# Optimization experiments

Hardware: AMD Instinct MI355X
Metric: run time of the kernel (lower is better)

The kernel has to match this reference:

```python
import jax, jax.numpy as jnp
import numpy as np

B = 2048; IN_DIM = 60; TTL = 30; H = 512; L = 5; OUT = 23
T_PTS = 90; SUB = 10  # fixed-step RK4 substeps per day (stands in for per-sample dopri5)
P_D = 0.2; P_H = 0.15; P_V = 0.25  # DELPHI fixed detection/hospitalization/ventilation fractions
LN2 = float(np.log(2.0))
R_I = LN2/5.0; R_D = LN2/2.0; R_RI = LN2/10.0; R_RH = LN2/15.0; R_RV = LN2/10.0


def setup_inputs():
    ks = jax.random.split(jax.random.key(0), 24)
    w = lambda k, s: (jax.random.normal(k, s) * 0.05).astype(jnp.float32)
    rng = jnp.array([1.0]*11 + [1.0, 60.0, 4.0, 0.5, 0.3, 0.5, 5.0, 5.0, 2.0, 60.0, 30.0, 1.0], dtype=jnp.float32)
    return {
        'model_input': jax.random.normal(ks[0], (B, IN_DIM), dtype=jnp.float32),
        'population': jax.random.uniform(ks[1], (B,), minval=1e5, maxval=1e7, dtype=jnp.float32),
        'cumulative_case_number': jax.random.uniform(ks[2], (B, 1), minval=1e3, maxval=1e5, dtype=jnp.float32),
        'mortality_rate': jax.random.uniform(ks[3], (B,), minval=0.01, maxval=0.05, dtype=jnp.float32),
        'h0': jax.random.normal(ks[4], (L, B, H), dtype=jnp.float32),
        'c0': jax.random.normal(ks[5], (L, B, H), dtype=jnp.float32),
        'W_ih0': w(ks[6], (4*H, TTL)),
        'W_ihR': w(ks[7], (L-1, 4*H, H)),
        'W_hh': w(ks[8], (L, 4*H, H)),
        'b_ih': w(ks[9], (L, 4*H)),
        'b_hh': w(ks[10], (L, 4*H)),
        'meta_W1': w(ks[11], (H, IN_DIM - TTL)), 'meta_b1': w(ks[12], (H,)),
        'meta_W2': w(ks[13], (H, H)), 'meta_b2': w(ks[14], (H,)),
        'ro_W1': w(ks[15], (2*H, 2*H)), 'ro_b1': w(ks[16], (2*H,)),
        'ro_W2': w(ks[17], (OUT, 2*H)), 'ro_b2': w(ks[18], (OUT,)),
        'dnn_output_range': rng,
        'sigmoid_scale': 1,
    }


def _backbone(model_input, population, h0, c0, W_ih0, W_ihR, W_hh, b_ih, b_hh,
              meta_W1, meta_b1, meta_W2, meta_b2, ro_W1, ro_b1, ro_W2, ro_b2,
              dnn_output_range, sigmoid_scale):
    x = model_input[:, :TTL] / population[:, None]
    for l in range(L):  # single-timestep, 5-layer LSTM; torch gate order i,f,g,o
        Wi = W_ih0 if l == 0 else W_ihR[l-1]
        g = x @ Wi.T + b_ih[l] + h0[l] @ W_hh[l].T + b_hh[l]
        gi, gf, gg, go = jnp.split(g, 4, axis=1)
        c = jax.nn.sigmoid(gf) * c0[l] + jax.nn.sigmoid(gi) * jnp.tanh(gg)
        x = jax.nn.sigmoid(go) * jnp.tanh(c)
    ts_out = x  # [B, H]
    m = jax.nn.relu(model_input[:, TTL:] @ meta_W1.T + meta_b1)
    m = jax.nn.relu(m @ meta_W2.T + meta_b2)
    z = jnp.concatenate([ts_out, m], axis=1)  # [B, 2H]
    z = jnp.tanh(z @ ro_W1.T + ro_b1)
    raw = z @ ro_W2.T + ro_b2  # [B, OUT]
    dnn = jax.nn.sigmoid(raw * sigmoid_scale) * dnn_output_range
    return dnn, ts_out, raw


def _ode(dnn, population, cumulative_case_number, mortality_rate):
    p = dnn[:, 11:]  # 12 fitted DELPHI params per sample
    alpha, days, r_s, r_dth, p_dth, r_dthdecay, k1, k2, jump, t_jump, std_normal, k3 = [p[:, j] for j in range(12)]
    N = population
    PopI = cumulative_case_number[:, 0]
    PopD = jnp.floor(mortality_rate * PopI)
    R_0 = jnp.where(PopI - PopD > 5.0 * PopD, 5.0 * PopD, 0.0)
    PopCI = PopI - PopD - R_0
    # DELPHI initial conditions
    S0 = N - (PopCI/P_D)*(k1 + k2) - R_0/P_D - PopD/P_D
    y0 = jnp.stack([
        S0,
        PopCI/P_D*k1,                      # E
        PopCI/P_D*k2,                      # I
        (PopCI/P_D - PopCI)*(1.0 - p_dth), # AR
        PopCI*P_H*(1.0 - p_dth),           # DHR
        PopCI*(1.0 - P_H)*(1.0 - p_dth),   # DQR
        (PopCI/P_D - PopCI)*p_dth,         # AD
        PopCI*P_H*p_dth,                   # DHD
        PopCI*(1.0 - P_H)*p_dth,           # DQD
        R_0/P_D,                           # R
        PopD/P_D,                          # D
        PopCI*P_H,                         # TH
        PopCI*P_H*P_V*(1.0 - p_dth),       # DVR
        PopCI*P_H*P_V*p_dth,               # DVD
        PopD,                              # DD
        PopI,                              # DT
    ], axis=1)  # [B, 16]

    def deriv(t, y):
        S, E, I = y[:, 0], y[:, 1], y[:, 2]
        AR, DHR, DQR, AD, DHD, DQD = y[:, 3], y[:, 4], y[:, 5], y[:, 6], y[:, 7], y[:, 8]
        DVR, DVD = y[:, 12], y[:, 13]
        gam = (2.0/jnp.pi)*jnp.arctan(-(t - days)/20.0*r_s) + 1.0 \
              + jump*jnp.exp(-(t - t_jump)**2/(2.0*std_normal**2))
        pdt = (2.0/jnp.pi)*(p_dth - 0.001)*(jnp.arctan(-t*r_dthdecay/20.0) + jnp.pi/2.0) + 0.001
        inf = alpha*gam*S*I/N
        det = R_D*I
        return jnp.stack([
            -inf,
            inf - R_I*E,
            R_I*E - det,
            det*(1.0-pdt)*(1.0-P_D) - R_RI*AR,
            det*(1.0-pdt)*P_D*P_H - R_RH*DHR,
            det*(1.0-pdt)*P_D*(1.0-P_H) - R_RI*DQR,
            det*pdt*(1.0-P_D) - r_dth*AD,
            det*pdt*P_D*P_H - r_dth*DHD,
            det*pdt*P_D*(1.0-P_H) - r_dth*DQD,
            R_RI*(AR + DQR) + R_RH*DHR,
            r_dth*(AD + DQD + DHD),
            det*P_D*P_H,
            det*(1.0-pdt)*P_D*P_H*P_V - R_RV*DVR,
            det*pdt*P_D*P_H*P_V - r_dth*DVD,
            r_dth*(DHD + DQD),
            det*P_D,
        ], axis=1)

    dt = 1.0 / SUB

    def segment(y, t0):
        def sub(yy, j):
            t = t0 + j*dt
            k1_ = deriv(t, yy)
            k2_ = deriv(t + 0.5*dt, yy + 0.5*dt*k1_)
            k3_ = deriv(t + 0.5*dt, yy + 0.5*dt*k2_)
            k4_ = deriv(t + dt, yy + dt*k3_)
            return yy + (dt/6.0)*(k1_ + 2.0*k2_ + 2.0*k3_ + k4_), None
        y2, _ = jax.lax.scan(sub, y, jnp.arange(SUB, dtype=jnp.float32))
        return y2, y2

    _, ys = jax.lax.scan(segment, y0, jnp.arange(T_PTS - 1, dtype=jnp.float32))
    sol = jnp.concatenate([y0[None], ys], axis=0)  # [T_PTS, B, 16]
    return jnp.transpose(sol, (1, 0, 2))  # [B, T_PTS, 16]


def reference(model_input, population, cumulative_case_number, mortality_rate, h0, c0,
              W_ih0, W_ihR, W_hh, b_ih, b_hh, meta_W1, meta_b1, meta_W2, meta_b2,
              ro_W1, ro_b1, ro_W2, ro_b2, dnn_output_range, sigmoid_scale):
    dnn, ts_out, raw = _backbone(model_input, population, h0, c0, W_ih0, W_ihR, W_hh,
                                 b_ih, b_hh, meta_W1, meta_b1, meta_W2, meta_b2,
                                 ro_W1, ro_b1, ro_W2, ro_b2, dnn_output_range, sigmoid_scale)
    sol = _ode(dnn, population, cumulative_case_number, mortality_rate)
    return sol, dnn, ts_out[:, None, :], raw
```

## Files before the change

### kernel.cpp

```cpp
#include <hip/hip_runtime.h>
#include <hip/hip_bf16.h>
#include <math.h>

#define BATCH 2048
#define HID 512
#define TPTS 90
#define NSEG 89
#define NSUB 10
#define NSTEPS 890

__device__ __constant__ const float kR_I  = 0.6931471805599453f / 5.0f;
__device__ __constant__ const float kR_D  = 0.6931471805599453f / 2.0f;
__device__ __constant__ const float kR_RI = 0.6931471805599453f / 10.0f;
__device__ __constant__ const float kR_RH = 0.6931471805599453f / 15.0f;
__device__ __constant__ const float kR_RV = 0.6931471805599453f / 10.0f;

typedef __attribute__((ext_vector_type(8))) short short8;
typedef __attribute__((ext_vector_type(4))) short short4v;
typedef __attribute__((ext_vector_type(4))) float float4v;

__device__ __forceinline__ float sigmoidf_(float x) { return 1.0f / (1.0f + expf(-x)); }

__global__ void prep_pad(const float* __restrict__ mi, const float* __restrict__ pop,
                         const float* __restrict__ Wih0, const float* __restrict__ mW1,
                         float* __restrict__ x0p, float* __restrict__ xmp,
                         float* __restrict__ Wp0, float* __restrict__ Wpm)
{
    int i = blockIdx.x * 256 + threadIdx.x;
    int r = i >> 5, c = i & 31;
    bool v = (c < 30);
    x0p[i] = v ? mi[r * 60 + c] / pop[r] : 0.0f;
    xmp[i] = v ? mi[r * 60 + 30 + c] : 0.0f;
    Wp0[i] = v ? Wih0[r * 30 + c] : 0.0f;
    if (r < 512) Wpm[i] = v ? mW1[r * 30 + c] : 0.0f;
}

template<bool WMODE>
__global__ void pack_split4(const float* __restrict__ s1, int ld1, int K1,
                            const float* __restrict__ s2, int ld2, int K2,
                            __hip_bfloat16* __restrict__ dst, int rows)
{
    int idx = blockIdx.x * 256 + threadIdx.x;
    int Ks = K1 + K2, Kq = Ks >> 2;
    if (idx >= rows * Kq) return;
    int r = idx / Kq, k4 = (idx - r * Kq) << 2;
    const float* srcp; int base, seg, kk;
    if (k4 < K1) { srcp = s1 + (size_t)r * ld1 + k4; base = 0; seg = K1; kk = k4; }
    else { kk = k4 - K1; srcp = s2 + (size_t)r * ld2 + kk; base = 3 * K1; seg = K2; }
    float4 x = *(const float4*)srcp;
    union { __hip_bfloat16 b[4]; short4v v; } H, L;
    H.b[0] = __float2bfloat16(x.x); H.b[1] = __float2bfloat16(x.y);
    H.b[2] = __float2bfloat16(x.z); H.b[3] = __float2bfloat16(x.w);
    L.b[0] = __float2bfloat16(x.x - __bfloat162float(H.b[0]));
    L.b[1] = __float2bfloat16(x.y - __bfloat162float(H.b[1]));
    L.b[2] = __float2bfloat16(x.z - __bfloat162float(H.b[2]));
    L.b[3] = __float2bfloat16(x.w - __bfloat162float(H.b[3]));
    __hip_bfloat16* d = dst + (size_t)r * (3 * Ks) + base;
    *(short4v*)(d + kk)           = H.v;
    *(short4v*)(d + seg + kk)     = WMODE ? L.v : H.v;
    *(short4v*)(d + 2 * seg + kk) = WMODE ? H.v : L.v;
}

template<int ACT>
__global__ __launch_bounds__(256)
void gemm_mfma(const __hip_bfloat16* __restrict__ Ah,
               const __hip_bfloat16* __restrict__ Wh, int K3,
               const float* __restrict__ b1, const float* __restrict__ b2,
               float* __restrict__ Cp, int ldc, int N)
{
    __shared__ __hip_bfloat16 As[128 * 32];
    __shared__ __hip_bfloat16 Ws[128 * 32];
    const int tid  = threadIdx.x;
    const int m0   = blockIdx.y * 128;
    const int n0   = blockIdx.x * 128;
    const int lane = tid & 63, wv = tid >> 6;
    const int mw   = (wv >> 1) * 64, nw = (wv & 1) * 64;
    const int l15  = lane & 15, quad = lane >> 4;
    const int sr   = tid >> 2;
    const int sc   = (tid & 3) * 8;

    float4v acc[4][4];
    #pragma unroll
    for (int i = 0; i < 4; ++i)
        #pragma unroll
        for (int j = 0; j < 4; ++j)
            acc[i][j] = (float4v){0.0f, 0.0f, 0.0f, 0.0f};

    const __hip_bfloat16* pa0 = Ah + (size_t)(m0 + sr)      * K3 + sc;
    const __hip_bfloat16* pa1 = Ah + (size_t)(m0 + sr + 64) * K3 + sc;
    const __hip_bfloat16* pw0 = Wh + (size_t)(n0 + sr)      * K3 + sc;
    const __hip_bfloat16* pw1 = Wh + (size_t)(n0 + sr + 64) * K3 + sc;

    short8 a0 = *(const short8*)(pa0);
    short8 a1 = *(const short8*)(pa1);
    short8 w0 = *(const short8*)(pw0);
    short8 w1 = *(const short8*)(pw1);

    for (int kt = 0; kt < K3; kt += 32) {
        __syncthreads();
        *(short8*)(As + sr * 32 + sc)        = a0;
        *(short8*)(As + (sr + 64) * 32 + sc) = a1;
        *(short8*)(Ws + sr * 32 + sc)        = w0;
        *(short8*)(Ws + (sr + 64) * 32 + sc) = w1;
        __syncthreads();

        int kn = kt + 32;
        if (kn < K3) {
            a0 = *(const short8*)(pa0 + kn);
            a1 = *(const short8*)(pa1 + kn);
            w0 = *(const short8*)(pw0 + kn);
            w1 = *(const short8*)(pw1 + kn);
        }

        short8 af[4], bf[4];
        #pragma unroll
        for (int t = 0; t < 4; ++t) {
            af[t] = *(const short8*)(As + (mw + t * 16 + l15) * 32 + quad * 8);
            bf[t] = *(const short8*)(Ws + (nw + t * 16 + l15) * 32 + quad * 8);
        }
        #pragma unroll
        for (int i = 0; i < 4; ++i)
            #pragma unroll
            for (int j = 0; j < 4; ++j)
                acc[i][j] = __builtin_amdgcn_mfma_f32_16x16x32_bf16(af[i], bf[j], acc[i][j], 0, 0, 0);
    }

    #pragma unroll
    for (int j = 0; j < 4; ++j) {
        int col = n0 + nw + j * 16 + l15;
        float bias = b1[col] + (b2 ? b2[col] : 0.0f);
        #pragma unroll
        for (int i = 0; i < 4; ++i) {
            #pragma unroll
            for (int r = 0; r < 4; ++r) {
                int row = m0 + mw + i * 16 + quad * 4 + r;
                float v = acc[i][j][r] + bias;
                if (ACT == 1)      v = fmaxf(v, 0.0f);
                else if (ACT == 2) v = tanhf(v);
                Cp[(size_t)row * ldc + col] = v;
            }
        }
    }
}

template<int ACT>
__global__ __launch_bounds__(256)
void gemm_dual(const float* __restrict__ A1, int lda1,
               const float* __restrict__ W1, int ldw1, int K1,
               const float* __restrict__ A2, int lda2,
               const float* __restrict__ W2, int ldw2, int K2,
               const float* __restrict__ b1p, const float* __restrict__ b2p,
               float* __restrict__ Cp, int ldc, int N)
{
    __shared__ float As[8][128];
    __shared__ float Ws[8][128];
    const int tid  = threadIdx.x;
    const int m0   = blockIdx.y * 128;
    const int n0   = blockIdx.x * 128;
    const int tm   = tid >> 4;
    const int tn   = tid & 15;
    const int lrow = tid >> 1;
    const int lkh  = (tid & 1) << 2;
    const int wrow = n0 + lrow;
    const int Ktot = K1 + K2;

    float acc[8][8];
    #pragma unroll
    for (int i = 0; i < 8; ++i)
        #pragma unroll
        for (int j = 0; j < 8; ++j) acc[i][j] = 0.0f;

    float4 av = *(const float4*)(A1 + (size_t)(m0 + lrow) * lda1 + lkh);
    float4 wv = make_float4(0.0f, 0.0f, 0.0f, 0.0f);
    if (wrow < N) wv = *(const float4*)(W1 + (size_t)wrow * ldw1 + lkh);

    for (int kt = 0; kt < Ktot; kt += 8) {
        __syncthreads();
        As[lkh + 0][lrow] = av.x; As[lkh + 1][lrow] = av.y;
        As[lkh + 2][lrow] = av.z; As[lkh + 3][lrow] = av.w;
        Ws[lkh + 0][lrow] = wv.x; Ws[lkh + 1][lrow] = wv.y;
        Ws[lkh + 2][lrow] = wv.z; Ws[lkh + 3][lrow] = wv.w;
        __syncthreads();

        int kn = kt + 8;
        float4 avn = make_float4(0.0f, 0.0f, 0.0f, 0.0f);
        float4 wvn = avn;
        if (kn < Ktot) {
            if (kn < K1) {
                avn = *(const float4*)(A1 + (size_t)(m0 + lrow) * lda1 + kn + lkh);
                if (wrow < N) wvn = *(const float4*)(W1 + (size_t)wrow * ldw1 + kn + lkh);
            } else {
                int k2 = kn - K1;
                avn = *(const float4*)(A2 + (size_t)(m0 + lrow) * lda2 + k2 + lkh);
                if (wrow < N) wvn = *(const float4*)(W2 + (size_t)wrow * ldw2 + k2 + lkh);
            }
        }

        #pragma unroll
        for (int kk = 0; kk < 8; ++kk) {
            float af[8], wf[8];
            #pragma unroll
            for (int i = 0; i < 4; ++i) {
                af[i]     = As[kk][tm * 8 + i];
                af[i + 4] = As[kk][tm * 8 + 4 + i];
                wf[i]     = Ws[kk][tn * 4 + i];
                wf[i + 4] = Ws[kk][64 + tn * 4 + i];
            }
            #pragma unroll
            for (int i = 0; i < 8; ++i)
                #pragma unroll
                for (int j = 0; j < 8; ++j)
                    acc[i][j] += af[i] * wf[j];
        }
        av = avn; wv = wvn;
    }

    #pragma unroll
    for (int j = 0; j < 8; ++j) {
        int col = n0 + ((j < 4) ? (tn * 4 + j) : (64 + tn * 4 + (j - 4)));
        if (col >= N) continue;
        float bias = b1p[col] + (b2p ? b2p[col] : 0.0f);
        #pragma unroll
        for (int i = 0; i < 8; ++i) {
            int rrow = m0 + tm * 8 + i;
            float v = acc[i][j] + bias;
            if (ACT == 1) v = fmaxf(v, 0.0f);
            else if (ACT == 2) v = tanhf(v);
            Cp[(size_t)rrow * ldc + col] = v;
        }
    }
}

__global__ __launch_bounds__(256)
void gemv_ro2(const float* __restrict__ A, const float* __restrict__ W,
              const float* __restrict__ b, float* __restrict__ C)
{
    int m    = blockIdx.x * 4 + (threadIdx.x >> 6);
    int lane = threadIdx.x & 63;
    const float* ar = A + (size_t)m * 1024 + lane * 4;
    float4 a0 = *(const float4*)(ar);
    float4 a1 = *(const float4*)(ar + 256);
    float4 a2 = *(const float4*)(ar + 512);
    float4 a3 = *(const float4*)(ar + 768);
    #pragma unroll 1
    for (int n = 0; n < 23; ++n) {
        const float* wr = W + (size_t)n * 1024 + lane * 4;
        float4 w0 = *(const float4*)(wr);
        float4 w1 = *(const float4*)(wr + 256);
        float4 w2 = *(const float4*)(wr + 512);
        float4 w3 = *(const float4*)(wr + 768);
        float s = a0.x * w0.x + a0.y * w0.y + a0.z * w0.z + a0.w * w0.w
                + a1.x * w1.x + a1.y * w1.y + a1.z * w1.z + a1.w * w1.w
                + a2.x * w2.x + a2.y * w2.y + a2.z * w2.z + a2.w * w2.w
                + a3.x * w3.x + a3.y * w3.y + a3.z * w3.z + a3.w * w3.w;
        #pragma unroll
        for (int o = 32; o > 0; o >>= 1) s += __shfl_xor(s, o, 64);
        if (lane == 0) C[m * 23 + n] = s + b[n];
    }
}

__global__ void lstm_gates(const float* __restrict__ G_, const float* __restrict__ c0l,
                           float* __restrict__ xout, int xld, float* __restrict__ ts)
{
    int i = blockIdx.x * 256 + threadIdx.x;
    int m = i >> 9, h = i & 511;
    const float* g = G_ + (size_t)m * 2048 + h;
    float gi = g[0], gf = g[512], gg = g[1024], go = g[1536];
    float c = sigmoidf_(gf) * c0l[i] + sigmoidf_(gi) * tanhf(gg);
    float x = sigmoidf_(go) * tanhf(c);
    xout[(size_t)m * xld + h] = x;
    if (ts) ts[i] = x;
}

__global__ void dnn_kernel(const float* __restrict__ raw, const int* __restrict__ ssp,
                           const float* __restrict__ rng, float* __restrict__ dnn)
{
    int i = blockIdx.x * 256 + threadIdx.x;
    if (i >= 2048 * 23) return;
    int c = i % 23;
    int v = *ssp;
    float ss = (v > 100000 || v < 0) ? __int_as_float(v) : (float)v;
    dnn[i] = sigmoidf_(raw[i] * ss) * rng[c];
}

__device__ __forceinline__ void gampdt_eval(float t, float alpha, float days, float rs20,
                                            float jump, float t_jump, float inv2s2,
                                            float pconst, float rdd20, float* ag, float* pd)
{
    float dtj = t - t_jump;
    float g = 0.6366197723675814f * atanf((days - t) * rs20) + 1.0f + jump * expf(-(dtj * dtj) * inv2s2);
    *ag = alpha * g;
    *pd = pconst * (atanf(-t * rdd20) + 1.5707963267948966f) + 0.001f;
}

__global__ void gampdt4_kernel(const float* __restrict__ dnn, const float* __restrict__ pop,
                               float4* __restrict__ ag4)
{
    int idx = blockIdx.x * 256 + threadIdx.x;
    if (idx >= NSTEPS * 2048) return;
    int e = idx & 2047;
    int k = idx >> 11;
    int s = k / 10, j = k - s * 10;
    const float* p = dnn + e * 23 + 11;
    float alpha = p[0], days = p[1], r_s = p[2], p_dth = p[4], r_dthdecay = p[5];
    float jump = p[8], t_jump = p[9], stdn = p[10];
    float invN = 1.0f / pop[e];
    float rs20   = r_s * 0.05f;
    float rdd20  = r_dthdecay * 0.05f;
    float inv2s2 = 1.0f / (2.0f * stdn * stdn);
    float pconst = 0.6366197723675814f * (p_dth - 0.001f);
    float t = (float)s + (float)j * 0.1f;
    float agh, pdh, ag1, pd1;
    gampdt_eval(t + 0.05f, alpha, days, rs20, jump, t_jump, inv2s2, pconst, rdd20, &agh, &pdh);
    gampdt_eval(t + 0.1f,  alpha, days, rs20, jump, t_jump, inv2s2, pconst, rdd20, &ag1, &pd1);
    ag4[idx] = make_float4(agh * invN, pdh, ag1 * invN, pd1);
}

__global__ __launch_bounds__(64)
void ode_core(const float* __restrict__ dnn, const float* __restrict__ pop,
              const float* __restrict__ ccn, const float* __restrict__ mort,
              const float4* __restrict__ ag4, float4* __restrict__ det4,
              float* __restrict__ sol)
{
    int e = blockIdx.x * 64 + threadIdx.x;
    const float* p = dnn + e * 23 + 11;
    float alpha = p[0], days = p[1], r_s = p[2], k1p = p[6], k2p = p[7];
    float jump = p[8], t_jump = p[9], stdn = p[10], p_dth = p[4], rdd = p[5];

    float N = pop[e];
    float invN = 1.0f / N;
    float PopI = ccn[e];
    float PopD = floorf(mort[e] * PopI);
    float R0v  = (PopI - PopD > 5.0f * PopD) ? 5.0f * PopD : 0.0f;
    float PopCI = PopI - PopD - R0v;
    float DP = PopCI / 0.2f;

    float y0 = N - DP * (k1p + k2p) - R0v / 0.2f - PopD / 0.2f;
    float y1 = DP * k1p;
    float y2 = DP * k2p;
    float y11 = PopCI * 0.15f;
    float y15 = PopI;

    float* sole = sol + (size_t)e * (TPTS * 16);
    sole[0] = y0; sole[1] = y1; sole[2] = y2; sole[11] = y11; sole[15] = y15;

    float rs20   = r_s * 0.05f;
    float rdd20  = rdd * 0.05f;
    float inv2s2 = 1.0f / (2.0f * stdn * stdn);
    float pconst = 0.6366197723675814f * (p_dth - 0.001f);
    float ag0, pd0;
    gampdt_eval(0.0f, alpha, days, rs20, jump, t_jump, inv2s2, pconst, rdd20, &ag0, &pd0);
    float agI = ag0 * invN;

    float4 cv[10];
    #pragma unroll
    for (int j = 0; j < 10; ++j) cv[j] = ag4[(size_t)j * 2048 + e];

    const float h6 = 0.016666668f;
    for (int s = 0; s < NSEG; ++s) {
        float Sdet = 0.0f;
        #pragma unroll
        for (int j = 0; j < 10; ++j) {
            float agh = cv[j].x, ag1 = cv[j].z;
            int kn = (s + 1) * 10 + j;
            if (kn >= NSTEPS) kn = NSTEPS - 1;
            cv[j] = ag4[(size_t)kn * 2048 + e];

            float det1 = kR_D * y2;
            float t1   = kR_I * y1;
            float inf  = agI * y0 * y2;
            float d1 = inf - t1, d2 = t1 - det1;
            float a0 = -inf, a1 = d1, a2 = d2;
            float z0 = y0 - 0.05f * inf, z1 = y1 + 0.05f * d1, z2 = y2 + 0.05f * d2;
            float det2 = kR_D * z2; t1 = kR_I * z1; inf = agh * z0 * z2;
            d1 = inf - t1; d2 = t1 - det2;
            a0 -= 2.0f * inf; a1 += 2.0f * d1; a2 += 2.0f * d2;
            z0 = y0 - 0.05f * inf; z1 = y1 + 0.05f * d1; z2 = y2 + 0.05f * d2;
            float det3 = kR_D * z2; t1 = kR_I * z1; inf = agh * z0 * z2;
            d1 = inf - t1; d2 = t1 - det3;
            a0 -= 2.0f * inf; a1 += 2.0f * d1; a2 += 2.0f * d2;
            z0 = y0 - 0.1f * inf; z1 = y1 + 0.1f * d1; z2 = y2 + 0.1f * d2;
            float det4v = kR_D * z2; t1 = kR_I * z1; inf = ag1 * z0 * z2;
            d1 = inf - t1; d2 = t1 - det4v;
            a0 -= inf; a1 += d1; a2 += d2;

            y0 += h6 * a0; y1 += h6 * a1; y2 += h6 * a2;
            float Wd = det1;
            Wd += 2.0f * det2; Wd += 2.0f * det3; Wd += det4v;
            Sdet += Wd;
            det4[(size_t)(s * 10 + j) * 2048 + e] = make_float4(det1, det2, det3, det4v);
            agI = ag1;
        }
        y11 += h6 * (0.03f * Sdet);
        y15 += h6 * (0.2f * Sdet);
        float* sp = sole + (size_t)(s + 1) * 16;
        sp[0] = y0; sp[1] = y1; sp[2] = y2; sp[11] = y11; sp[15] = y15;
    }
}

__global__ __launch_bounds__(64)
void ode_decay(const float* __restrict__ dnn, const float* __restrict__ ccn,
               const float* __restrict__ mort, const float4* __restrict__ ag4,
               const float4* __restrict__ det4, float* __restrict__ sol)
{
    const int t  = blockIdx.x * 64 + threadIdx.x;
    const int e  = t >> 3;
    const int g  = t & 7;
    const int lane = threadIdx.x & 63;
    const int base = lane & ~7;

    const float* p = dnn + e * 23 + 11;
    float r_dth = p[3], p_dth = p[4];

    float PopI = ccn[e];
    float PopD = floorf(mort[e] * PopI);
    float R0v  = (PopI - PopD > 5.0f * PopD) ? 5.0f * PopD : 0.0f;
    float PopCI = PopI - PopD - R0v;
    float DP = PopCI / 0.2f;
    float ompd = 1.0f - p_dth;

    float iy3  = (DP - PopCI) * ompd;
    float iy4  = PopCI * 0.15f * ompd;
    float iy5  = PopCI * 0.85f * ompd;
    float iy6  = (DP - PopCI) * p_dth;
    float iy7  = PopCI * 0.15f * p_dth;
    float iy8  = PopCI * 0.85f * p_dth;
    float iy12 = PopCI * 0.15f * 0.25f * ompd;
    float iy13 = PopCI * 0.15f * 0.25f * p_dth;

    float ha = (g == 0) ? iy3 : (g == 1) ? iy4 : (g == 2) ? iy5 : iy6;
    float hb = (g == 4) ? iy7 : (g == 5) ? iy8 : (g == 6) ? iy12 : iy13;
    float ys = (g < 4) ? ha : hb;
    float c1 = (g == 0) ? 0.8f : (g == 1) ? 0.03f : (g == 2) ? 0.17f : (g == 6) ? 0.0075f : 0.0f;
    float c2 = (g == 3) ? 0.8f : (g == 4) ? 0.03f : (g == 5) ? 0.17f : (g == 7) ? 0.0075f : 0.0f;
    float rr = (g == 0 || g == 2) ? kR_RI : (g == 1) ? kR_RH : (g == 6) ? kR_RV : r_dth;
    int own_idx = (g < 4) ? ((g < 2) ? (g == 0 ? 3 : 4) : (g == 2 ? 5 : 6))
                          : ((g < 6) ? (g == 4 ? 7 : 8) : (g == 6 ? 12 : 13));

    float y9  = R0v / 0.2f;
    float y10 = PopD / 0.2f;
    float y14 = PopD;

    float* sole = sol + (size_t)e * (TPTS * 16);
    sole[own_idx] = ys;
    if (g == 0) sole[9]  = y9;
    if (g == 1) sole[10] = y10;
    if (g == 2) sole[14] = y14;

    float pconst = 0.6366197723675814f * (p_dth - 0.001f);
    float pd0 = pconst * 1.5707963267948966f + 0.001f;
    float u0 = c1 * (1.0f - pd0) + c2 * pd0;

    float4 cvd[10], cva[10];
    #pragma unroll
    for (int j = 0; j < 10; ++j) {
        cvd[j] = det4[(size_t)j * 2048 + e];
        cva[j] = ag4[(size_t)j * 2048 + e];
    }

    const float h6 = 0.016666668f;
    for (int s = 0; s < NSEG; ++s) {
        float Sy = 0.0f;
        #pragma unroll
        for (int j = 0; j < 10; ++j) {
            float4 dd = cvd[j];
            float pdh = cva[j].y, pd1 = cva[j].w;
            int kn = (s + 1) * 10 + j;
            if (kn >= NSTEPS) kn = NSTEPS - 1;
            cvd[j] = det4[(size_t)kn * 2048 + e];
            cva[j] = ag4[(size_t)kn * 2048 + e];

            float uh = c1 * (1.0f - pdh) + c2 * pdh;
            float u1 = c1 * (1.0f - pd1) + c2 * pd1;
            float k1v = dd.x * u0 - rr * ys;
            float zs1 = ys + 0.05f * k1v;
            float k2v = dd.y * uh - rr * zs1;
            float zs2 = ys + 0.05f * k2v;
            float k3v = dd.z * uh - rr * zs2;
            float zs3 = ys + 0.1f * k3v;
            float k4v = dd.w * u1 - rr * zs3;
            float ka = k1v + 2.0f * (k2v + k3v) + k4v;
            Sy += ys + 2.0f * (zs1 + zs2) + zs3;
            ys += h6 * ka;
            u0 = u1;
        }
        float S0 = __shfl(Sy, base + 0, 64);
        float S1 = __shfl(Sy, base + 1, 64);
        float S2 = __shfl(Sy, base + 2, 64);
        float S3 = __shfl(Sy, base + 3, 64);
        float S4 = __shfl(Sy, base + 4, 64);
        float S5 = __shfl(Sy, base + 5, 64);
        y9  += h6 * (kR_RI * (S0 + S2) + kR_RH * S1);
        y10 += h6 * (r_dth * ((S3 + S4) + S5));
        y14 += h6 * (r_dth * (S4 + S5));

        float* sp = sole + (size_t)(s + 1) * 16;
        sp[own_idx] = ys;
        if (g == 0) sp[9]  = y9;
        if (g == 1) sp[10] = y10;
        if (g == 2) sp[14] = y14;
    }
}

__device__ __forceinline__ void deriv16(const float* y, float ag, float pd,
                                        float invN, float r_dth, float* d)
{
    float inf = ag * y[0] * y[2] * invN;
    float det = kR_D * y[2];
    float t1  = kR_I * y[1];
    float omp = 1.0f - pd;
    float dq  = det * omp;
    float dp  = det * pd;
    float dq003 = dq * 0.03f;
    float dp003 = dp * 0.03f;
    d[0]  = -inf;
    d[1]  = inf - t1;
    d[2]  = t1 - det;
    d[3]  = dq * 0.8f  - kR_RI * y[3];
    d[4]  = dq003      - kR_RH * y[4];
    d[5]  = dq * 0.17f - kR_RI * y[5];
    d[6]  = dp * 0.8f  - r_dth * y[6];
    d[7]  = dp003      - r_dth * y[7];
    d[8]  = dp * 0.17f - r_dth * y[8];
    d[9]  = kR_RI * (y[3] + y[5]) + kR_RH * y[4];
    d[10] = r_dth * ((y[6] + y[7]) + y[8]);
    d[11] = det * 0.03f;
    d[12] = 0.25f * dq003 - kR_RV * y[12];
    d[13] = 0.25f * dp003 - r_dth * y[13];
    d[14] = r_dth * (y[7] + y[8]);
    d[15] = det * 0.2f;
}

__global__ __launch_bounds__(64)
void ode_kernel(const float* __restrict__ dnn, const float* __restrict__ pop,
                const float* __restrict__ ccn, const float* __restrict__ mort,
                float* __restrict__ sol)
{
    int e = blockIdx.x * 64 + threadIdx.x;
    const float* p = dnn + e * 23 + 11;
    float alpha = p[0], days = p[1], r_s = p[2], r_dth = p[3], p_dth = p[4];
    float r_dthdecay = p[5], k1p = p[6], k2p = p[7], jump = p[8], t_jump = p[9], stdn = p[10];

    float N = pop[e];
    float invN = 1.0f / N;
    float PopI = ccn[e];
    float PopD = floorf(mort[e] * PopI);
    float R0v  = (PopI - PopD > 5.0f * PopD) ? 5.0f * PopD : 0.0f;
    float PopCI = PopI - PopD - R0v;
    float DP = PopCI / 0.2f;

    float y[16];
    y[0]  = N - DP * (k1p + k2p) - R0v / 0.2f - PopD / 0.2f;
    y[1]  = DP * k1p;
    y[2]  = DP * k2p;
    y[3]  = (DP - PopCI) * (1.0f - p_dth);
    y[4]  = PopCI * 0.15f * (1.0f - p_dth);
    y[5]  = PopCI * 0.85f * (1.0f - p_dth);
    y[6]  = (DP - PopCI) * p_dth;
    y[7]  = PopCI * 0.15f * p_dth;
    y[8]  = PopCI * 0.85f * p_dth;
    y[9]  = R0v / 0.2f;
    y[10] = PopD / 0.2f;
    y[11] = PopCI * 0.15f;
    y[12] = PopCI * 0.15f * 0.25f * (1.0f - p_dth);
    y[13] = PopCI * 0.15f * 0.25f * p_dth;
    y[14] = PopD;
    y[15] = PopI;

    {
        float* sp = sol + (size_t)e * (TPTS * 16);
        #pragma unroll
        for (int i = 0; i < 16; ++i) sp[i] = y[i];
    }

    float rs20   = r_s * 0.05f;
    float rdd20  = r_dthdecay * 0.05f;
    float inv2s2 = 1.0f / (2.0f * stdn * stdn);
    float pconst = 0.6366197723675814f * (p_dth - 0.001f);

    float ag0, pd0;
    gampdt_eval(0.0f, alpha, days, rs20, jump, t_jump, inv2s2, pconst, rdd20, &ag0, &pd0);

    for (int s = 0; s < NSEG; ++s) {
        float t0 = (float)s;
        for (int j = 0; j < NSUB; ++j) {
            float agh, pdh, ag1, pd1;
            float t = t0 + (float)j * 0.1f;
            gampdt_eval(t + 0.05f, alpha, days, rs20, jump, t_jump, inv2s2, pconst, rdd20, &agh, &pdh);
            gampdt_eval(t + 0.1f,  alpha, days, rs20, jump, t_jump, inv2s2, pconst, rdd20, &ag1, &pd1);
            float d[16], acc[16], yt[16];
            deriv16(y, ag0, pd0, invN, r_dth, d);
            #pragma unroll
            for (int i = 0; i < 16; ++i) { acc[i] = d[i]; yt[i] = y[i] + 0.05f * d[i]; }
            deriv16(yt, agh, pdh, invN, r_dth, d);
            #pragma unroll
            for (int i = 0; i < 16; ++i) { acc[i] += 2.0f * d[i]; yt[i] = y[i] + 0.05f * d[i]; }
            deriv16(yt, agh, pdh, invN, r_dth, d);
            #pragma unroll
            for (int i = 0; i < 16; ++i) { acc[i] += 2.0f * d[i]; yt[i] = y[i] + 0.1f * d[i]; }
            deriv16(yt, ag1, pd1, invN, r_dth, d);
            #pragma unroll
            for (int i = 0; i < 16; ++i) y[i] += 0.016666668f * (acc[i] + d[i]);
            ag0 = ag1; pd0 = pd1;
        }
        float* sp = sol + (size_t)e * (TPTS * 16) + (size_t)(s + 1) * 16;
        #pragma unroll
        for (int i = 0; i < 16; ++i) sp[i] = y[i];
    }
}

extern "C" void kernel_launch(void* const* d_in, const int* in_sizes, int n_in,
                              void* d_out, int out_size, void* d_ws, size_t ws_size,
                              hipStream_t stream)
{
    const float* mi   = (const float*)d_in[0];
    const float* pop  = (const float*)d_in[1];
    const float* ccn  = (const float*)d_in[2];
    const float* mort = (const float*)d_in[3];
    const float* h0   = (const float*)d_in[4];
    const float* c0   = (const float*)d_in[5];
    const float* Wih0 = (const float*)d_in[6];
    const float* WihR = (const float*)d_in[7];
    const float* Whh  = (const float*)d_in[8];
    const float* bih  = (const float*)d_in[9];
    const float* bhh  = (const float*)d_in[10];
    const float* mW1  = (const float*)d_in[11];
    const float* mb1  = (const float*)d_in[12];
    const float* mW2  = (const float*)d_in[13];
    const float* mb2  = (const float*)d_in[14];
    const float* rW1  = (const float*)d_in[15];
    const float* rb1  = (const float*)d_in[16];
    const float* rW2  = (const float*)d_in[17];
    const float* rb2  = (const float*)d_in[18];
    const float* rng  = (const float*)d_in[19];
    const int*   ssp  = (const int*)d_in[20];

    float* out   = (float*)d_out;
    float* sol_o = out;
    float* dnn_o = out + 2949120;
    float* ts_o  = out + 2949120 + 47104;
    float* raw_o = out + 2949120 + 47104 + 1048576;

    float* ws  = (float*)d_ws;
    float* G   = ws;
    float* Z   = ws + 4194304;
    float* X0  = ws + 6291456;
    float* X1  = ws + 7340032;
    float* x0p = ws + 8388608;
    float* xmp = ws + 8454144;
    float* Wp0 = ws + 8519680;
    float* Wpm = ws + 8585216;
    __hip_bfloat16* Ab = (__hip_bfloat16*)(ws + 8601600);
    __hip_bfloat16* Wb = (__hip_bfloat16*)(ws + 8601600 + 3145728);
    float4* AG4  = (float4*)(ws + 8601600);
    float4* DET4 = (float4*)ws;
    bool wsOK = ws_size >= (size_t)15892480 * sizeof(float);

    prep_pad<<<256, 256, 0, stream>>>(mi, pop, Wih0, mW1, x0p, xmp, Wp0, Wpm);

    gemm_dual<1><<<dim3(4, 16), 256, 0, stream>>>(xmp, 32, Wpm, 32, 32,
                                                  nullptr, 0, nullptr, 0, 0,
                                                  mb1, nullptr, G, 512, 512);

    if (wsOK) {
        pack_split4<false><<<(2048 * 128 + 255) / 256, 256, 0, stream>>>(G, 512, 512, nullptr, 0, 0, Ab, 2048);
        pack_split4<true ><<<(512  * 128 + 255) / 256, 256, 0, stream>>>(mW2, 512, 512, nullptr, 0, 0, Wb, 512);
        gemm_mfma<1><<<dim3(4, 16), 256, 0, stream>>>(Ab, Wb, 1536, mb2, nullptr, Z + 512, 1024, 512);

        for (int l = 0; l < 5; ++l) {
            const float* A1 = (l == 0) ? x0p : ((l & 1) ? X1 : X0);
            int          K1 = (l == 0) ? 32 : 512;
            const float* W1 = (l == 0) ? Wp0 : (WihR + (size_t)(l - 1) * 1048576);
            int Ks = K1 + 512, K3 = 3 * Ks, Kq = Ks >> 2;
            pack_split4<false><<<(2048 * Kq + 255) / 256, 256, 0, stream>>>(
                A1, K1, K1, h0 + (size_t)l * 1048576, 512, 512, Ab, 2048);
            pack_split4<true ><<<(2048 * Kq + 255) / 256, 256, 0, stream>>>(
                W1, K1, K1, Whh + (size_t)l * 1048576, 512, 512, Wb, 2048);
            gemm_mfma<0><<<dim3(16, 16), 256, 0, stream>>>(
                Ab, Wb, K3, bih + l * 2048, bhh + l * 2048, G, 2048, 2048);
            float* xo  = (l == 4) ? Z : ((l & 1) ? X0 : X1);
            int    xol = (l == 4) ? 1024 : 512;
            lstm_gates<<<4096, 256, 0, stream>>>(G, c0 + (size_t)l * 1048576, xo, xol,
                                                 (l == 4) ? ts_o : nullptr);
        }

        pack_split4<false><<<(2048 * 256 + 255) / 256, 256, 0, stream>>>(Z, 1024, 1024, nullptr, 0, 0, Ab, 2048);
        pack_split4<true ><<<(1024 * 256 + 255) / 256, 256, 0, stream>>>(rW1, 1024, 1024, nullptr, 0, 0, Wb, 1024);
        gemm_mfma<2><<<dim3(8, 16), 256, 0, stream>>>(Ab, Wb, 3072, rb1, nullptr, G, 1024, 1024);
    } else {
        gemm_dual<1><<<dim3(4, 16), 256, 0, stream>>>(G, 512, mW2, 512, 512,
                                                      nullptr, 0, nullptr, 0, 0,
                                                      mb2, nullptr, Z + 512, 1024, 512);
        for (int l = 0; l < 5; ++l) {
            const float* A1 = (l == 0) ? x0p : ((l & 1) ? X1 : X0);
            int          K1 = (l == 0) ? 32 : 512;
            const float* W1 = (l == 0) ? Wp0 : (WihR + (size_t)(l - 1) * 1048576);
            gemm_dual<0><<<dim3(16, 16), 256, 0, stream>>>(
                A1, K1, W1, K1, K1,
                h0 + (size_t)l * 1048576, 512, Whh + (size_t)l * 1048576, 512, 512,
                bih + l * 2048, bhh + l * 2048, G, 2048, 2048);
            float* xo  = (l == 4) ? Z : ((l & 1) ? X0 : X1);
            int    xol = (l == 4) ? 1024 : 512;
            lstm_gates<<<4096, 256, 0, stream>>>(G, c0 + (size_t)l * 1048576, xo, xol,
                                                 (l == 4) ? ts_o : nullptr);
        }
        gemm_dual<2><<<dim3(8, 16), 256, 0, stream>>>(Z, 1024, rW1, 1024, 1024,
                                                      nullptr, 0, nullptr, 0, 0,
                                                      rb1, nullptr, G, 1024, 1024);
    }

    gemv_ro2<<<512, 256, 0, stream>>>(G, rW2, rb2, raw_o);
    dnn_kernel<<<184, 256, 0, stream>>>(raw_o, ssp, rng, dnn_o);

    if (wsOK) {
        gampdt4_kernel<<<(NSTEPS * 2048 + 255) / 256, 256, 0, stream>>>(dnn_o, pop, AG4);
        ode_core<<<32, 64, 0, stream>>>(dnn_o, pop, ccn, mort, AG4, DET4, sol_o);
        ode_decay<<<256, 64, 0, stream>>>(dnn_o, ccn, mort, AG4, DET4, sol_o);
    } else {
        ode_kernel<<<32, 64, 0, stream>>>(dnn_o, pop, ccn, mort, sol_o);
    }
    (void)in_sizes; (void)n_in; (void)out_size;
}
```

Baseline: 812.6 us.

## Fuse pack launches, shrink GEMM tile, use direct global-to-LDS loads, fuse dnn epilogue

The A and W bf16 split-packing kernels are merged into one launch per GEMM. The MFMA GEMM tile is narrowed from 128x128 to 128x64, which doubles the grid and adds an occupancy hint. When the builtin is available, tiles are loaded with global_load_lds straight into shared memory, dropping the register-staged prefetch. The sigmoid/range output step is folded into the readout GEMV, removing a separate kernel. Together these cut launch overhead and try to improve GEMM occupancy, at the cost of losing the software prefetch overlap and adding more redundant A-tile reads.

```diff
diff --git a/kernel.cpp b/kernel.cpp
--- a/kernel.cpp
+++ b/kernel.cpp
@@ -9,6 +9,15 @@
 #define NSUB 10
 #define NSTEPS 890
 
+#if defined(__has_builtin)
+#if __has_builtin(__builtin_amdgcn_global_load_lds)
+#define HAS_GLL 1
+#endif
+#endif
+#ifndef HAS_GLL
+#define HAS_GLL 0
+#endif
+
 __device__ __constant__ const float kR_I  = 0.6931471805599453f / 5.0f;
 __device__ __constant__ const float kR_D  = 0.6931471805599453f / 2.0f;
 __device__ __constant__ const float kR_RI = 0.6931471805599453f / 10.0f;
@@ -20,6 +29,14 @@
 typedef __attribute__((ext_vector_type(4))) float float4v;
 
 __device__ __forceinline__ float sigmoidf_(float x) { return 1.0f / (1.0f + expf(-x)); }
+
+#if HAS_GLL
+__device__ __forceinline__ void gll16(const void* g, void* l) {
+    __builtin_amdgcn_global_load_lds(
+        (const __attribute__((address_space(1))) unsigned int*)g,
+        (__attribute__((address_space(3))) unsigned int*)l, 16, 0, 0);
+}
+#endif
 
 __global__ void prep_pad(const float* __restrict__ mi, const float* __restrict__ pop,
                          const float* __restrict__ Wih0, const float* __restrict__ mW1,
@@ -35,14 +52,11 @@
     if (r < 512) Wpm[i] = v ? mW1[r * 30 + c] : 0.0f;
 }
 
-template<bool WMODE>
-__global__ void pack_split4(const float* __restrict__ s1, int ld1, int K1,
-                            const float* __restrict__ s2, int ld2, int K2,
-                            __hip_bfloat16* __restrict__ dst, int rows)
-{
-    int idx = blockIdx.x * 256 + threadIdx.x;
+__device__ __forceinline__ void pack_quad(const float* __restrict__ s1, int ld1, int K1,
+                                          const float* __restrict__ s2, int ld2, int K2,
+                                          __hip_bfloat16* __restrict__ dst, int idx, bool wm)
+{
     int Ks = K1 + K2, Kq = Ks >> 2;
-    if (idx >= rows * Kq) return;
     int r = idx / Kq, k4 = (idx - r * Kq) << 2;
     const float* srcp; int base, seg, kk;
     if (k4 < K1) { srcp = s1 + (size_t)r * ld1 + k4; base = 0; seg = K1; kk = k4; }
@@ -57,76 +71,105 @@
     L.b[3] = __float2bfloat16(x.w - __bfloat162float(H.b[3]));
     __hip_bfloat16* d = dst + (size_t)r * (3 * Ks) + base;
     *(short4v*)(d + kk)           = H.v;
-    *(short4v*)(d + seg + kk)     = WMODE ? L.v : H.v;
-    *(short4v*)(d + 2 * seg + kk) = WMODE ? H.v : L.v;
+    *(short4v*)(d + seg + kk)     = wm ? L.v : H.v;
+    *(short4v*)(d + 2 * seg + kk) = wm ? H.v : L.v;
+}
+
+__global__ void pack_pair(const float* __restrict__ a1, int alda1, int aK1,
+                          const float* __restrict__ a2, int alda2, int aK2,
+                          __hip_bfloat16* __restrict__ da, int arows,
+                          const float* __restrict__ w1, int wld1, int wK1,
+                          const float* __restrict__ w2, int wld2, int wK2,
+                          __hip_bfloat16* __restrict__ dw, int wrows)
+{
+    int aKq = (aK1 + aK2) >> 2, wKq = (wK1 + wK2) >> 2;
+    int qa = arows * aKq;
+    int idx = blockIdx.x * 256 + threadIdx.x;
+    if (idx < qa) {
+        pack_quad(a1, alda1, aK1, a2, alda2, aK2, da, idx, false);
+    } else {
+        idx -= qa;
+        if (idx < wrows * wKq) pack_quad(w1, wld1, wK1, w2, wld2, wK2, dw, idx, true);
+    }
 }
 
 template<int ACT>
-__global__ __launch_bounds__(256)
+__global__ __launch_bounds__(256, 2)
 void gemm_mfma(const __hip_bfloat16* __restrict__ Ah,
                const __hip_bfloat16* __restrict__ Wh, int K3,
                const float* __restrict__ b1, const float* __restrict__ b2,
                float* __restrict__ Cp, int ldc, int N)
 {
     __shared__ __hip_bfloat16 As[128 * 32];
-    __shared__ __hip_bfloat16 Ws[128 * 32];
+    __shared__ __hip_bfloat16 Ws[64 * 32];
     const int tid  = threadIdx.x;
     const int m0   = blockIdx.y * 128;
-    const int n0   = blockIdx.x * 128;
+    const int n0   = blockIdx.x * 64;
     const int lane = tid & 63, wv = tid >> 6;
-    const int mw   = (wv >> 1) * 64, nw = (wv & 1) * 64;
+    const int mw   = (wv >> 1) * 64, nw = (wv & 1) * 32;
     const int l15  = lane & 15, quad = lane >> 4;
     const int sr   = tid >> 2;
     const int sc   = (tid & 3) * 8;
 
-    float4v acc[4][4];
+    float4v acc[4][2];
     #pragma unroll
     for (int i = 0; i < 4; ++i)
         #pragma unroll
-        for (int j = 0; j < 4; ++j)
+        for (int j = 0; j < 2; ++j)
             acc[i][j] = (float4v){0.0f, 0.0f, 0.0f, 0.0f};
 
     const __hip_bfloat16* pa0 = Ah + (size_t)(m0 + sr)      * K3 + sc;
     const __hip_bfloat16* pa1 = Ah + (size_t)(m0 + sr + 64) * K3 + sc;
     const __hip_bfloat16* pw0 = Wh + (size_t)(n0 + sr)      * K3 + sc;
-    const __hip_bfloat16* pw1 = Wh + (size_t)(n0 + sr + 64) * K3 + sc;
-
+
+#if HAS_GLL
+    char* ldsA0 = (char*)As + wv * 1024;
+    char* ldsA1 = (char*)As + 4096 + wv * 1024;
+    char* ldsW0 = (char*)Ws + wv * 1024;
+#endif
+
+#if !HAS_GLL
     short8 a0 = *(const short8*)(pa0);
     short8 a1 = *(const short8*)(pa1);
     short8 w0 = *(const short8*)(pw0);
-    short8 w1 = *(const short8*)(pw1);
+#endif
 
     for (int kt = 0; kt < K3; kt += 32) {
+#if HAS_GLL
+        __syncthreads();
+        gll16(pa0 + kt, ldsA0);
+        gll16(pa1 + kt, ldsA1);
+        gll16(pw0 + kt, ldsW0);
+        __syncthreads();
+#else
         __syncthreads();
         *(short8*)(As + sr * 32 + sc)        = a0;
         *(short8*)(As + (sr + 64) * 32 + sc) = a1;
         *(short8*)(Ws + sr * 32 + sc)        = w0;
-        *(short8*)(Ws + (sr + 64) * 32 + sc) = w1;
         __syncthreads();
-
         int kn = kt + 32;
         if (kn < K3) {
             a0 = *(const short8*)(pa0 + kn);
             a1 = *(const short8*)(pa1 + kn);
             w0 = *(const short8*)(pw0 + kn);
-            w1 = *(const short8*)(pw1 + kn);
-        }
-
-        short8 af[4], bf[4];
-        #pragma unroll
-        for (int t = 0; t < 4; ++t) {
+        }
+#endif
+        short8 af[4], bf[2];
+        #pragma unroll
+        for (int t = 0; t < 4; ++t)
             af[t] = *(const short8*)(As + (mw + t * 16 + l15) * 32 + quad * 8);
+        #pragma unroll
+        for (int t = 0; t < 2; ++t)
             bf[t] = *(const short8*)(Ws + (nw + t * 16 + l15) * 32 + quad * 8);
-        }
         #pragma unroll
         for (int i = 0; i < 4; ++i)
             #pragma unroll
-            for (int j = 0; j < 4; ++j)
+            for (int j = 0; j < 2; ++j)
                 acc[i][j] = __builtin_amdgcn_mfma_f32_16x16x32_bf16(af[i], bf[j], acc[i][j], 0, 0, 0);
     }
 
     #pragma unroll
-    for (int j = 0; j < 4; ++j) {
+    for (int j = 0; j < 2; ++j) {
         int col = n0 + nw + j * 16 + l15;
         float bias = b1[col] + (b2 ? b2[col] : 0.0f);
         #pragma unroll
@@ -233,7 +276,9 @@
 
 __global__ __launch_bounds__(256)
 void gemv_ro2(const float* __restrict__ A, const float* __restrict__ W,
-              const float* __restrict__ b, float* __restrict__ C)
+              const float* __restrict__ b, const int* __restrict__ ssp,
+              const float* __restrict__ rng, float* __restrict__ raw,
+              float* __restrict__ dnn)
 {
     int m    = blockIdx.x * 4 + (threadIdx.x >> 6);
     int lane = threadIdx.x & 63;
@@ -242,6 +287,8 @@
     float4 a1 = *(const float4*)(ar + 256);
     float4 a2 = *(const float4*)(ar + 512);
     float4 a3 = *(const float4*)(ar + 768);
+    int v = *ssp;
+    float ss = (v > 100000 || v < 0) ? __int_as_float(v) : (float)v;
     #pragma unroll 1
     for (int n = 0; n < 23; ++n) {
         const float* wr = W + (size_t)n * 1024 + lane * 4;
@@ -255,7 +302,11 @@
                 + a3.x * w3.x + a3.y * w3.y + a3.z * w3.z + a3.w * w3.w;
         #pragma unroll
         for (int o = 32; o > 0; o >>= 1) s += __shfl_xor(s, o, 64);
-        if (lane == 0) C[m * 23 + n] = s + b[n];
+        if (lane == 0) {
+            float r2 = s + b[n];
+            raw[m * 23 + n] = r2;
+            dnn[m * 23 + n] = sigmoidf_(r2 * ss) * rng[n];
+        }
     }
 }
 
@@ -663,20 +714,20 @@
                                                   mb1, nullptr, G, 512, 512);
 
     if (wsOK) {
-        pack_split4<false><<<(2048 * 128 + 255) / 256, 256, 0, stream>>>(G, 512, 512, nullptr, 0, 0, Ab, 2048);
-        pack_split4<true ><<<(512  * 128 + 255) / 256, 256, 0, stream>>>(mW2, 512, 512, nullptr, 0, 0, Wb, 512);
-        gemm_mfma<1><<<dim3(4, 16), 256, 0, stream>>>(Ab, Wb, 1536, mb2, nullptr, Z + 512, 1024, 512);
+        pack_pair<<<(2048 * 128 + 512 * 128 + 255) / 256, 256, 0, stream>>>(
+            G, 512, 512, nullptr, 0, 0, Ab, 2048,
+            mW2, 512, 512, nullptr, 0, 0, Wb, 512);
+        gemm_mfma<1><<<dim3(8, 16), 256, 0, stream>>>(Ab, Wb, 1536, mb2, nullptr, Z + 512, 1024, 512);
 
         for (int l = 0; l < 5; ++l) {
             const float* A1 = (l == 0) ? x0p : ((l & 1) ? X1 : X0);
             int          K1 = (l == 0) ? 32 : 512;
             const float* W1 = (l == 0) ? Wp0 : (WihR + (size_t)(l - 1) * 1048576);
             int Ks = K1 + 512, K3 = 3 * Ks, Kq = Ks >> 2;
-            pack_split4<false><<<(2048 * Kq + 255) / 256, 256, 0, stream>>>(
-                A1, K1, K1, h0 + (size_t)l * 1048576, 512, 512, Ab, 2048);
-            pack_split4<true ><<<(2048 * Kq + 255) / 256, 256, 0, stream>>>(
+            pack_pair<<<(2048 * Kq * 2 + 255) / 256, 256, 0, stream>>>(
+                A1, K1, K1, h0 + (size_t)l * 1048576, 512, 512, Ab, 2048,
                 W1, K1, K1, Whh + (size_t)l * 1048576, 512, 512, Wb, 2048);
-            gemm_mfma<0><<<dim3(16, 16), 256, 0, stream>>>(
+            gemm_mfma<0><<<dim3(32, 16), 256, 0, stream>>>(
                 Ab, Wb, K3, bih + l * 2048, bhh + l * 2048, G, 2048, 2048);
             float* xo  = (l == 4) ? Z : ((l & 1) ? X0 : X1);
             int    xol = (l == 4) ? 1024 : 512;
@@ -684,9 +735,16 @@
                                                  (l == 4) ? ts_o : nullptr);
         }
 
-        pack_split4<false><<<(2048 * 256 + 255) / 256, 256, 0, stream>>>(Z, 1024, 1024, nullptr, 0, 0, Ab, 2048);
-        pack_split4<true ><<<(1024 * 256 + 255) / 256, 256, 0, stream>>>(rW1, 1024, 1024, nullptr, 0, 0, Wb, 1024);
-        gemm_mfma<2><<<dim3(8, 16), 256, 0, stream>>>(Ab, Wb, 3072, rb1, nullptr, G, 1024, 1024);
+        pack_pair<<<(2048 * 256 + 1024 * 256 + 255) / 256, 256, 0, stream>>>(
+            Z, 1024, 1024, nullptr, 0, 0, Ab, 2048,
+            rW1, 1024, 1024, nullptr, 0, 0, Wb, 1024);
+        gemm_mfma<2><<<dim3(16, 16), 256, 0, stream>>>(Ab, Wb, 3072, rb1, nullptr, G, 1024, 1024);
+
+        gemv_ro2<<<512, 256, 0, stream>>>(G, rW2, rb2, ssp, rng, raw_o, dnn_o);
+
+        gampdt4_kernel<<<(NSTEPS * 2048 + 255) / 256, 256, 0, stream>>>(dnn_o, pop, AG4);
+        ode_core<<<32, 64, 0, stream>>>(dnn_o, pop, ccn, mort, AG4, DET4, sol_o);
+        ode_decay<<<256, 64, 0, stream>>>(dnn_o, ccn, mort, AG4, DET4, sol_o);
     } else {
         gemm_dual<1><<<dim3(4, 16), 256, 0, stream>>>(G, 512, mW2, 512, 512,
                                                       nullptr, 0, nullptr, 0, 0,
@@ -707,16 +765,10 @@
         gemm_dual<2><<<dim3(8, 16), 256, 0, stream>>>(Z, 1024, rW1, 1024, 1024,
                                                       nullptr, 0, nullptr, 0, 0,
                                                       rb1, nullptr, G, 1024, 1024);
-    }
-
-    gemv_ro2<<<512, 256, 0, stream>>>(G, rW2, rb2, raw_o);
-    dnn_kernel<<<184, 256, 0, stream>>>(raw_o, ssp, rng, dnn_o);
-
-    if (wsOK) {
-        gampdt4_kernel<<<(NSTEPS * 2048 + 255) / 256, 256, 0, stream>>>(dnn_o, pop, AG4);
-        ode_core<<<32, 64, 0, stream>>>(dnn_o, pop, ccn, mort, AG4, DET4, sol_o);
-        ode_decay<<<256, 64, 0, stream>>>(dnn_o, ccn, mort, AG4, DET4, sol_o);
-    } else {
+        gemm_dual<0><<<dim3(1, 16), 256, 0, stream>>>(G, 1024, rW2, 1024, 1024,
+                                                      nullptr, 0, nullptr, 0, 0,
+                                                      rb2, nullptr, raw_o, 23, 23);
+        dnn_kernel<<<184, 256, 0, stream>>>(raw_o, ssp, rng, dnn_o);
         ode_kernel<<<32, 64, 0, stream>>>(dnn_o, pop, ccn, mort, sol_o);
     }
     (void)in_sizes; (void)n_in; (void)out_size;
```

Result: faster. 794.7 us (-2.2%).
